# Kernel tuning notes

Hardware: AMD Instinct MI355X
Metric: run time of the kernel (lower is better)

Reference implementation:

```python
import jax, jax.numpy as jnp
import numpy as np
import math

# ---- sizes (must match setup_inputs) ----
D = 256          # distribution dim
K = 2 * D        # parameters per embedding: mean + hidden (log) variance
L = 64           # classes present in batch
B = 8            # samples per class (B_total = B*L = 512)
S = 16           # config['sample_size']
C = 64           # num_classes
LOG_EPS = -100.0
LOG2PI = math.log(2.0 * math.pi)

# ---- NormalDistribution (diagonal, exp parametrization) helpers ----

def _split(p):
    # (..., K) -> mean (..., D), hidden log-variance (..., D)
    return p[..., :D], p[..., D:]


def _logpdf(params, x):
    m, h = _split(params)
    return -0.5 * jnp.sum(LOG2PI + h + (x - m) ** 2 * jnp.exp(-h), axis=-1)


def _logmls(p1, p2):
    # log int N(x; m1, v1) N(x; m2, v2) dx = log N(m1; m2, v1 + v2)
    m1, h1 = _split(p1)
    m2, h2 = _split(p2)
    v = jnp.exp(h1) + jnp.exp(h2)
    return -0.5 * jnp.sum(LOG2PI + jnp.log(v) + (m1 - m2) ** 2 / v, axis=-1)


def _pdf_product(p1, p2):
    # product of two diagonal Gaussians -> new Gaussian params (broadcasting)
    m1, h1 = _split(p1)
    m2, h2 = _split(p2)
    v1, v2 = jnp.exp(h1), jnp.exp(h2)
    vs = v1 + v2
    v = v1 * v2 / vs
    m = (m1 * v2 + m2 * v1) / vs
    return jnp.concatenate(jnp.broadcast_arrays(m, jnp.log(v)), axis=-1)


def _prototypes(support, eps_var):
    # support: (B2, L, K) -> fused prototype params (L, K)
    m, h = _split(support)
    v = eps_var + jnp.exp(h)            # (B2, L, D)
    inv = 1.0 / v
    new_var = 1.0 / inv.sum(0)          # (L, D)
    new_mean = new_var * (m * inv).sum(0)
    new_h = jnp.log(eps_var + new_var)  # ipositive(variance + new_var)
    return jnp.concatenate([new_mean, new_h], axis=-1)


def _compute_logits(query, support, eps_var, key):
    # query: (b, L, K); support: (b2, L, K) -> logits (b, L, L)
    b = query.shape[0]
    protos = _prototypes(support, eps_var)                      # (L, K)
    p = _pdf_product(query[:, :, None, :], protos[None, None])  # (b, L, L, K)
    m, h = _split(p)
    eps = jax.random.normal(key, (b, L, S, L, D), dtype=query.dtype)
    samples = m[:, :, None] + jnp.exp(0.5 * h[:, :, None]) * eps  # (b, L, S, L, D)
    lm = _logmls(query[:, :, None, :], protos[None, None])        # (b, L, L)
    tl = _logpdf(protos[None, None, None], samples)               # (b, L, S, L)
    lse = jax.scipy.special.logsumexp(tl, axis=-1, keepdims=True)  # (b, L, S, 1)
    return lm + jax.scipy.special.logsumexp(-lse, axis=-2) - math.log(S)


def _group_by_class(parameters, labels):
    # balanced labels: each of L labels appears exactly B times
    idx = jnp.argsort(labels)                 # stable in jax
    order = idx.reshape(L, B).T               # (B, L): i-th occurrence of each label
    label_map = labels[idx].reshape(L, B)[:, 0]
    by_class = parameters[idx].reshape(L, B, K).transpose(1, 0, 2)  # (B, L, K)
    return by_class, order, label_map


def setup_inputs() -> dict:
    key = jax.random.key(0)
    k1, k2 = jax.random.split(key)
    parameters = jax.random.normal(k1, (B * L, K), dtype=jnp.float32)
    # balanced labels: each class in [0, L) appears exactly B times, shuffled
    labels = jax.random.permutation(k2, jnp.arange(B * L, dtype=jnp.int32) % L).astype(jnp.int64)
    hidden_epsilon = jnp.asarray(0.01 ** (2.0 / D), dtype=jnp.float32)
    return {"parameters": parameters, "hidden_epsilon": hidden_epsilon, "labels": labels}


def reference(parameters, hidden_epsilon, labels):
    eps_var = jnp.exp(hidden_epsilon)
    by_class, order, label_map = _group_by_class(parameters, labels)
    k = B // 2
    key = jax.random.key(42)
    s1, s2 = jax.random.split(key)
    logits1 = _compute_logits(by_class[:k], by_class[k:], eps_var, s1)
    logits2 = _compute_logits(by_class[k:], by_class[:k], eps_var, s2)
    logits = jnp.concatenate([logits1, logits2], axis=0)          # (B, L, L)
    all_logits = jnp.full((B, L, C), LOG_EPS, dtype=logits.dtype)
    all_logits = all_logits.at[:, :, label_map].set(logits)       # scatter on class dim
    all_logits = all_logits.reshape(B * L, C)
    return all_logits[jnp.argsort(order.reshape(-1))]             # unsort to input order
```

## Files before the change

### kernel.cpp

```cpp
#include <hip/hip_runtime.h>
#include <math.h>

#define DD 256
#define KK 512
#define LL 64
#define BB 8
#define SS 16
#define F_LOG2PI 1.83787706641f
#define PER_I 16777216u

typedef float v2f __attribute__((ext_vector_type(2)));

struct U2 { unsigned x, y; };

__host__ __device__ constexpr U2 tf2x32(unsigned k0, unsigned k1, unsigned c0, unsigned c1) {
  unsigned ks2 = k0 ^ k1 ^ 0x1BD11BDAu;
  unsigned x0 = c0 + k0;
  unsigned x1 = c1 + k1;
#define TFR(r) { x0 += x1; x1 = (x1 << (r)) | (x1 >> (32 - (r))); x1 ^= x0; }
  TFR(13) TFR(15) TFR(26) TFR(6)   x0 += k1;  x1 += ks2 + 1u;
  TFR(17) TFR(29) TFR(16) TFR(24)  x0 += ks2; x1 += k0 + 2u;
  TFR(13) TFR(15) TFR(26) TFR(6)   x0 += k0;  x1 += k1 + 3u;
  TFR(17) TFR(29) TFR(16) TFR(24)  x0 += k1;  x1 += ks2 + 4u;
  TFR(13) TFR(15) TFR(26) TFR(6)   x0 += ks2; x1 += k0 + 5u;
#undef TFR
  return U2{x0, x1};
}

__device__ inline unsigned rotl(unsigned x, unsigned r) {
  return __builtin_amdgcn_alignbit(x, x, 32u - r);
}

__device__ inline unsigned tf_fold(unsigned k0, unsigned k1, unsigned x1) {
  unsigned ks2 = k0 ^ k1 ^ 0x1BD11BDAu;
  unsigned x0 = k0;
#define TFR(r) { x0 += x1; x1 = rotl(x1, r); x1 ^= x0; }
  TFR(13u) TFR(15u) TFR(26u) TFR(6u)   x0 += k1;  x1 += ks2 + 1u;
  TFR(17u) TFR(29u) TFR(16u) TFR(24u)  x0 += ks2; x1 += k0 + 2u;
  TFR(13u) TFR(15u) TFR(26u) TFR(6u)   x0 += k0;  x1 += k1 + 3u;
  TFR(17u) TFR(29u) TFR(16u) TFR(24u)  x0 += k1;  x1 += ks2 + 4u;
  TFR(13u) TFR(15u) TFR(26u) TFR(6u)   x0 += ks2; x1 += k0 + 5u;
#undef TFR
  return x0 ^ x1;
}

__device__ inline v2f pkfma(v2f a, v2f b, v2f c) {
#if __has_builtin(__builtin_elementwise_fma)
  return __builtin_elementwise_fma(a, b, c);
#else
  v2f r; r.x = fmaf(a.x, b.x, c.x); r.y = fmaf(a.y, b.y, c.y); return r;
#endif
}

__device__ inline float normal_pu(unsigned b) {
  float two_fp = __uint_as_float((b >> 9) | 0x40000000u);
  float u = fmaxf(-0.99999994f, two_fp - 3.0f);
  float w = -__logf(fmaf(-u, u, 1.0f));
  v2f ww; ww.x = w - 2.5f; ww.y = __builtin_amdgcn_sqrtf(w) - 3.0f;
  v2f p2; p2.x = 2.81022636e-08f; p2.y = -0.000200214257f;
  p2 = pkfma(p2, ww, (v2f){ 3.43273939e-07f,  0.000100950558f});
  p2 = pkfma(p2, ww, (v2f){-3.5233877e-06f,   0.00134934322f});
  p2 = pkfma(p2, ww, (v2f){-4.39150654e-06f, -0.00367342844f});
  p2 = pkfma(p2, ww, (v2f){ 0.00021858087f,   0.00573950773f});
  p2 = pkfma(p2, ww, (v2f){-0.00125372503f,  -0.0076224613f});
  p2 = pkfma(p2, ww, (v2f){-0.00417768164f,   0.00943887047f});
  p2 = pkfma(p2, ww, (v2f){ 0.246640727f,     1.00167406f});
  p2 = pkfma(p2, ww, (v2f){ 1.50140941f,      2.83297682f});
  float p = (w < 5.0f) ? p2.x : p2.y;
  return p * u;
}


__global__ void k_sort(const int* __restrict__ labels, int* __restrict__ pos,
                       int* __restrict__ lmap) {
  __shared__ int lab[512];
  __shared__ int cnt[64];
  __shared__ int mode;
  int t = threadIdx.x;
  int v = labels[t];
  if (t < 64) cnt[t] = 0;
  if (t == 0) mode = 0;
  __syncthreads();
  atomicAdd(&cnt[v & 63], 1);
  __syncthreads();
  if (t < 64 && cnt[t] != 8) mode = 1;
  __syncthreads();
  if (mode) v = labels[2 * t];
  lab[t] = v & 63;
  __syncthreads();
  int c = lab[t];
  int o = 0;
  for (int j = 0; j < t; ++j) o += (lab[j] == c);
  pos[c * 8 + o] = t;
  if (t < 64) lmap[t] = t;
}

__global__ void k_protos(const float* __restrict__ P, const float* __restrict__ he_p,
                         const int* __restrict__ pos, float4* __restrict__ pq,
                         float* __restrict__ cl, float4* __restrict__ accz) {
  int hb = blockIdx.x;
  int h = hb >> 6, l = hb & 63;
  int d = threadIdx.x;
  {
    float4 z; z.x = z.y = z.z = z.w = 0.0f;
    float4* base = accz + (hb * 256 + d) * 4;
#pragma unroll
    for (int j = 0; j < 4; ++j) base[j] = z;
  }
  float eps_var = expf(he_p[0]);
  int soff = h ? 0 : 4;
  float sinv = 0.f, sminv = 0.f;
#pragma unroll
  for (int j = 0; j < 4; ++j) {
    int row = pos[l * 8 + soff + j];
    float m = P[row * KK + d];
    float hh = P[row * KK + DD + d];
    float vv = eps_var + expf(hh);
    float iv = 1.0f / vv;
    sinv += iv; sminv += m * iv;
  }
  float nv = 1.0f / sinv;
  float nm = nv * sminv;
  float ev = eps_var + nv;
  float4 rec; rec.x = nm; rec.y = ev; rec.z = 1.0f / ev; rec.w = 0.0f;
  pq[(h * 256 + d) * 64 + l] = rec;
  float t = F_LOG2PI + __logf(ev);
  for (int off = 32; off; off >>= 1) t += __shfl_xor(t, off);
  __shared__ float red[4];
  int w = d >> 6, lane = d & 63;
  if (lane == 0) red[w] = t;
  __syncthreads();
  if (d == 0) cl[hb] = red[0] + red[1] + red[2] + red[3];
}

__global__ void k_lm(const float* __restrict__ P, const int* __restrict__ pos,
                     const float4* __restrict__ pq, float* __restrict__ lm) {
  int w = threadIdx.x >> 6, lane = threadIdx.x & 63;
  int bb = blockIdx.x * 4 + w;
  int g = bb >> 6, lq = bb & 63;
  int h = g >> 2;
  __shared__ float2 q[4][256];
  int row = pos[lq * 8 + g];
#pragma unroll
  for (int j = 0; j < 4; ++j) {
    int d = j * 64 + lane;
    float2 rec;
    rec.x = P[row * KK + d];
    rec.y = expf(P[row * KK + DD + d]);
    q[w][d] = rec;
  }
  const float4* pp = pq + h * 256 * 64 + lane;
  float t = 0.0f;
#pragma unroll 4
  for (int d = 0; d < 256; ++d) {
    float4 pr = pp[d * 64];
    float2 qv = q[w][d];
    float vs = qv.y + pr.y;
    float diff = qv.x - pr.x;
    t += __logf(vs) + diff * diff * __builtin_amdgcn_rcpf(vs);
  }
  lm[bb * 64 + lane] = -0.5f * (256.0f * F_LOG2PI + t);
}

__global__ __launch_bounds__(256) void k_tl(const float* __restrict__ P,
    const int* __restrict__ pos, const float4* __restrict__ pq,
    float* __restrict__ accbuf) {
  constexpr U2 S1 = tf2x32(0u, 42u, 0u, 0u);
  constexpr U2 S2 = tf2x32(0u, 42u, 0u, 1u);
  int bb = blockIdx.x;
  int h = bb >> 10;
  int lq = (bb >> 4) & 63;
  int chunk = bb & 15;
  int t = threadIdx.x;

  __shared__ float2 q[4 * 256];
#pragma unroll
  for (int i = 0; i < 4; ++i) {
    int row = pos[lq * 8 + h * 4 + i];
    float2 rec;
    rec.x = P[row * KK + t];
    rec.y = expf(P[row * KK + DD + t]);
    q[i * 256 + t] = rec;
  }
  __syncthreads();

  int w = t >> 6, lane = t & 63;
  unsigned k0 = h ? S2.x : S1.x;
  unsigned k1 = h ? S2.y : S1.y;
  unsigned ebk = (unsigned)w * PER_I + (unsigned)lq * 262144u +
                 (unsigned)lane * 256u + (unsigned)chunk * 16u + k1;
  const float2* qd = &q[w * 256];
  const float4* pp = pq + (h * 256 + chunk * 16) * 64 + lane;
  int g = h * 4 + w;
  float* dst = accbuf + ((g * 64 + lq) * 16) * 64 + lane;

  float acc[16];
#pragma unroll
  for (int s = 0; s < 16; ++s) acc[s] = 0.0f;

#pragma unroll 1
  for (int dd = 0; dd < 16; ++dd) {
    float4 pr = pp[dd * 64];
    float2 qv = qd[chunk * 16 + dd];
    float vs  = qv.y + pr.y;
    float ivs = __builtin_amdgcn_rcpf(vs);
    float evs = pr.y * ivs;
    float sivp = __builtin_amdgcn_sqrtf(pr.z);
    float A = (qv.x - pr.x) * evs * sivp;
    float S = __builtin_amdgcn_sqrtf(qv.y * evs) * sivp * 1.41421356f;
    unsigned ebkd = ebk + (unsigned)dd;
#pragma unroll
    for (int s = 0; s < 16; ++s) {
      unsigned bits = tf_fold(k0, k1, ebkd + (unsigned)s * 16384u);
      float eps = normal_pu(bits);
      float diff = fmaf(S, eps, A);
      acc[s] = fmaf(diff, diff, acc[s]);
    }
  }
#pragma unroll
  for (int s = 0; s < 16; ++s) atomicAdd(dst + s * 64, acc[s]);
}

__global__ void k_final(const float* __restrict__ lm, const float* __restrict__ accbuf,
                        const float* __restrict__ cl, const int* __restrict__ pos,
                        const int* __restrict__ lmap, float* __restrict__ out) {
  int bb = blockIdx.x;
  int g = bb >> 6, lq = bb & 63;
  int h = g >> 2;
  int t = threadIdx.x, w = t >> 6, lane = t & 63;
  __shared__ float lsebuf[16];
  float clv = cl[h * 64 + lane];
#pragma unroll
  for (int j = 0; j < 4; ++j) {
    int s = w * 4 + j;
    float tlv = -0.5f * (clv + accbuf[(bb * 16 + s) * 64 + lane]);
    float mx = tlv;
    for (int off = 32; off; off >>= 1) mx = fmaxf(mx, __shfl_xor(mx, off));
    float se = expf(tlv - mx);
    for (int off = 32; off; off >>= 1) se += __shfl_xor(se, off);
    if (lane == 0) lsebuf[s] = mx + __logf(se);
  }
  __syncthreads();
  if (t < 64) {
    float a = (t < 16) ? -lsebuf[t] : -INFINITY;
    float mx = a;
    for (int off = 32; off; off >>= 1) mx = fmaxf(mx, __shfl_xor(mx, off));
    float e = (t < 16) ? expf(a - mx) : 0.0f;
    for (int off = 32; off; off >>= 1) e += __shfl_xor(e, off);
    float mc = mx + __logf(e) - 2.7725887f;
    int row = pos[lq * 8 + g];
    out[row * 64 + lmap[t]] = lm[bb * 64 + t] + mc;
  }
}

extern "C" void kernel_launch(void* const* d_in, const int* in_sizes, int n_in,
                              void* d_out, int out_size, void* d_ws, size_t ws_size,
                              hipStream_t stream) {
  (void)in_sizes; (void)n_in; (void)out_size; (void)ws_size;
  const float* P      = (const float*)d_in[0];
  const float* he     = (const float*)d_in[1];
  const int*   labels = (const int*)d_in[2];
  float* out = (float*)d_out;

  float* ws = (float*)d_ws;
  float* accbuf = ws;
  float4* pq = (float4*)(ws + 524288);
  float* cl  = ws + 655360;
  float* lmw = ws + 655488;
  int*   pos = (int*)(ws + 688256);
  int*   lmp = pos + 512;

  hipLaunchKernelGGL(k_sort,   dim3(1),    dim3(512), 0, stream, labels, pos, lmp);
  hipLaunchKernelGGL(k_protos, dim3(128),  dim3(256), 0, stream, P, he, pos, pq, cl,
                     (float4*)accbuf);
  hipLaunchKernelGGL(k_lm,     dim3(128),  dim3(256), 0, stream, P, pos, pq, lmw);
  hipLaunchKernelGGL(k_tl,     dim3(2048), dim3(256), 0, stream, P, pos, pq, accbuf);
  hipLaunchKernelGGL(k_final,  dim3(512),  dim3(256), 0, stream, lmw, accbuf, cl, pos, lmp, out);
}
```

Baseline: 413.7 us.

## Fuse label sort into protos kernel and fold lm computation into k_tl

Every k_protos block now recomputes the label grouping redundantly in shared memory, and block 0 writes pos and lmap, so the single-block sort launch goes away. The logmls term is accumulated inside k_tl's per-dimension loop and reduced through atomics into a new buffer that k_protos zeroes, so the separate k_lm launch goes away too. This cuts five launches to three, but adds redundant sort work to every protos block and extra atomics to k_tl.

```diff
diff --git a/kernel.cpp b/kernel.cpp
--- a/kernel.cpp
+++ b/kernel.cpp
@@ -71,48 +71,58 @@
 }
 
 
-__global__ void k_sort(const int* __restrict__ labels, int* __restrict__ pos,
-                       int* __restrict__ lmap) {
+__global__ void k_protos(const float* __restrict__ P, const float* __restrict__ he_p,
+                         const int* __restrict__ labels, float4* __restrict__ pq,
+                         float* __restrict__ cl, float4* __restrict__ accz,
+                         float4* __restrict__ lmz, int* __restrict__ pos,
+                         int* __restrict__ lmap) {
+  int hb = blockIdx.x;
+  int h = hb >> 6, l = hb & 63;
+  int d = threadIdx.x;
+
+  {
+    float4 z; z.x = z.y = z.z = z.w = 0.0f;
+    float4* base = accz + (hb * 256 + d) * 4;
+#pragma unroll
+    for (int j = 0; j < 4; ++j) base[j] = z;
+    int gtid = hb * 256 + d;
+    if (gtid < 8192) lmz[gtid] = z;
+  }
+
   __shared__ int lab[512];
   __shared__ int cnt[64];
   __shared__ int mode;
-  int t = threadIdx.x;
-  int v = labels[t];
-  if (t < 64) cnt[t] = 0;
-  if (t == 0) mode = 0;
-  __syncthreads();
-  atomicAdd(&cnt[v & 63], 1);
-  __syncthreads();
-  if (t < 64 && cnt[t] != 8) mode = 1;
-  __syncthreads();
-  if (mode) v = labels[2 * t];
-  lab[t] = v & 63;
-  __syncthreads();
-  int c = lab[t];
-  int o = 0;
-  for (int j = 0; j < t; ++j) o += (lab[j] == c);
-  pos[c * 8 + o] = t;
-  if (t < 64) lmap[t] = t;
-}
-
-__global__ void k_protos(const float* __restrict__ P, const float* __restrict__ he_p,
-                         const int* __restrict__ pos, float4* __restrict__ pq,
-                         float* __restrict__ cl, float4* __restrict__ accz) {
-  int hb = blockIdx.x;
-  int h = hb >> 6, l = hb & 63;
-  int d = threadIdx.x;
-  {
-    float4 z; z.x = z.y = z.z = z.w = 0.0f;
-    float4* base = accz + (hb * 256 + d) * 4;
-#pragma unroll
-    for (int j = 0; j < 4; ++j) base[j] = z;
-  }
+  __shared__ int posl[512];
+  if (d < 64) cnt[d] = 0;
+  if (d == 0) mode = 0;
+  __syncthreads();
+  int v0 = labels[d], v1 = labels[d + 256];
+  atomicAdd(&cnt[v0 & 63], 1);
+  atomicAdd(&cnt[v1 & 63], 1);
+  __syncthreads();
+  if (d < 64 && cnt[d] != 8) mode = 1;
+  __syncthreads();
+  if (mode) { v0 = labels[2 * d]; v1 = labels[2 * (d + 256)]; }
+  lab[d] = v0 & 63; lab[d + 256] = v1 & 63;
+  __syncthreads();
+#pragma unroll
+  for (int e = d; e < 512; e += 256) {
+    int c = lab[e], o = 0;
+    for (int j = 0; j < e; ++j) o += (lab[j] == c);
+    posl[c * 8 + o] = e;
+  }
+  __syncthreads();
+  if (hb == 0) {
+    pos[d] = posl[d]; pos[d + 256] = posl[d + 256];
+    if (d < 64) lmap[d] = d;
+  }
+
   float eps_var = expf(he_p[0]);
   int soff = h ? 0 : 4;
   float sinv = 0.f, sminv = 0.f;
 #pragma unroll
   for (int j = 0; j < 4; ++j) {
-    int row = pos[l * 8 + soff + j];
+    int row = posl[l * 8 + soff + j];
     float m = P[row * KK + d];
     float hh = P[row * KK + DD + d];
     float vv = eps_var + expf(hh);
@@ -133,38 +143,9 @@
   if (d == 0) cl[hb] = red[0] + red[1] + red[2] + red[3];
 }
 
-__global__ void k_lm(const float* __restrict__ P, const int* __restrict__ pos,
-                     const float4* __restrict__ pq, float* __restrict__ lm) {
-  int w = threadIdx.x >> 6, lane = threadIdx.x & 63;
-  int bb = blockIdx.x * 4 + w;
-  int g = bb >> 6, lq = bb & 63;
-  int h = g >> 2;
-  __shared__ float2 q[4][256];
-  int row = pos[lq * 8 + g];
-#pragma unroll
-  for (int j = 0; j < 4; ++j) {
-    int d = j * 64 + lane;
-    float2 rec;
-    rec.x = P[row * KK + d];
-    rec.y = expf(P[row * KK + DD + d]);
-    q[w][d] = rec;
-  }
-  const float4* pp = pq + h * 256 * 64 + lane;
-  float t = 0.0f;
-#pragma unroll 4
-  for (int d = 0; d < 256; ++d) {
-    float4 pr = pp[d * 64];
-    float2 qv = q[w][d];
-    float vs = qv.y + pr.y;
-    float diff = qv.x - pr.x;
-    t += __logf(vs) + diff * diff * __builtin_amdgcn_rcpf(vs);
-  }
-  lm[bb * 64 + lane] = -0.5f * (256.0f * F_LOG2PI + t);
-}
-
 __global__ __launch_bounds__(256) void k_tl(const float* __restrict__ P,
     const int* __restrict__ pos, const float4* __restrict__ pq,
-    float* __restrict__ accbuf) {
+    float* __restrict__ accbuf, float* __restrict__ lmacc) {
   constexpr U2 S1 = tf2x32(0u, 42u, 0u, 0u);
   constexpr U2 S2 = tf2x32(0u, 42u, 0u, 1u);
   int bb = blockIdx.x;
@@ -197,6 +178,7 @@
   float acc[16];
 #pragma unroll
   for (int s = 0; s < 16; ++s) acc[s] = 0.0f;
+  float lmpart = 0.0f;
 
 #pragma unroll 1
   for (int dd = 0; dd < 16; ++dd) {
@@ -206,7 +188,9 @@
     float ivs = __builtin_amdgcn_rcpf(vs);
     float evs = pr.y * ivs;
     float sivp = __builtin_amdgcn_sqrtf(pr.z);
-    float A = (qv.x - pr.x) * evs * sivp;
+    float dif = qv.x - pr.x;
+    lmpart += __logf(vs) + dif * dif * ivs;
+    float A = dif * evs * sivp;
     float S = __builtin_amdgcn_sqrtf(qv.y * evs) * sivp * 1.41421356f;
     unsigned ebkd = ebk + (unsigned)dd;
 #pragma unroll
@@ -219,9 +203,10 @@
   }
 #pragma unroll
   for (int s = 0; s < 16; ++s) atomicAdd(dst + s * 64, acc[s]);
-}
-
-__global__ void k_final(const float* __restrict__ lm, const float* __restrict__ accbuf,
+  atomicAdd(lmacc + (g * 64 + lq) * 64 + lane, lmpart);
+}
+
+__global__ void k_final(const float* __restrict__ lmacc, const float* __restrict__ accbuf,
                         const float* __restrict__ cl, const int* __restrict__ pos,
                         const int* __restrict__ lmap, float* __restrict__ out) {
   int bb = blockIdx.x;
@@ -248,8 +233,9 @@
     float e = (t < 16) ? expf(a - mx) : 0.0f;
     for (int off = 32; off; off >>= 1) e += __shfl_xor(e, off);
     float mc = mx + __logf(e) - 2.7725887f;
+    float lmv = -0.5f * (256.0f * F_LOG2PI + lmacc[bb * 64 + t]);
     int row = pos[lq * 8 + g];
-    out[row * 64 + lmap[t]] = lm[bb * 64 + t] + mc;
+    out[row * 64 + lmap[t]] = lmv + mc;
   }
 }
 
@@ -264,16 +250,14 @@
 
   float* ws = (float*)d_ws;
   float* accbuf = ws;
-  float4* pq = (float4*)(ws + 524288);
-  float* cl  = ws + 655360;
-  float* lmw = ws + 655488;
+  float* lmacc  = ws + 524288;
+  float4* pq = (float4*)(ws + 557056);
+  float* cl  = ws + 688128;
   int*   pos = (int*)(ws + 688256);
   int*   lmp = pos + 512;
 
-  hipLaunchKernelGGL(k_sort,   dim3(1),    dim3(512), 0, stream, labels, pos, lmp);
-  hipLaunchKernelGGL(k_protos, dim3(128),  dim3(256), 0, stream, P, he, pos, pq, cl,
-                     (float4*)accbuf);
-  hipLaunchKernelGGL(k_lm,     dim3(128),  dim3(256), 0, stream, P, pos, pq, lmw);
-  hipLaunchKernelGGL(k_tl,     dim3(2048), dim3(256), 0, stream, P, pos, pq, accbuf);
-  hipLaunchKernelGGL(k_final,  dim3(512),  dim3(256), 0, stream, lmw, accbuf, cl, pos, lmp, out);
-}
+  hipLaunchKernelGGL(k_protos, dim3(128),  dim3(256), 0, stream, P, he, labels, pq, cl,
+                     (float4*)accbuf, (float4*)lmacc, pos, lmp);
+  hipLaunchKernelGGL(k_tl,     dim3(2048), dim3(256), 0, stream, P, pos, pq, accbuf, lmacc);
+  hipLaunchKernelGGL(k_final,  dim3(512),  dim3(256), 0, stream, lmacc, accbuf, cl, pos, lmp, out);
+}
```

Result: faster. 393.7 us, median of 2 (-4.8%).
